# Optimization experiments

Hardware: AMD Instinct MI355X
Metric: run time of the kernel (lower is better)

## Reference

```python
import jax, jax.numpy as jnp
import numpy as np

EPS_MSG = 1e-7
EPS_BN = 1e-5


def _seg_softmax(logits, seg, num_segments):
    # logits: [E, D] per-edge logits; softmax over edges sharing the same dst node
    m = jax.ops.segment_max(logits, seg, num_segments=num_segments)
    m = jnp.where(jnp.isfinite(m), m, 0.0)
    e = jnp.exp(logits - m[seg])
    s = jax.ops.segment_sum(e, seg, num_segments=num_segments)
    return e / (s[seg] + 1e-16)


def _batchnorm(h, gamma, beta):
    mu = jnp.mean(h, axis=0)
    var = jnp.var(h, axis=0)
    return (h - mu) * jax.lax.rsqrt(var + EPS_BN) * gamma + beta


def setup_inputs() -> dict:
    key = jax.random.key(0)
    ks = jax.random.split(key, 12)
    N, E, G, D, L = 100000, 600000, 512, 128, 7
    x = jax.random.randint(ks[0], (N, 9), 0, 64, dtype=jnp.int32)
    edge_index = jax.random.randint(ks[1], (2, E), 0, N, dtype=jnp.int32)
    edge_attr = jax.random.randint(ks[2], (E, 3), 0, 8, dtype=jnp.int32)
    batch = jnp.sort(jax.random.randint(ks[3], (N,), 0, G, dtype=jnp.int32))
    rf_pred = jax.random.uniform(ks[4], (G,), dtype=jnp.float32)
    atom_emb = jax.random.normal(ks[5], (9, 64, D), dtype=jnp.float32) * 0.02
    bond_emb = jax.random.normal(ks[6], (3, 8, D), dtype=jnp.float32) * 0.02
    conv_w = jax.random.normal(ks[7], (L, D, D), dtype=jnp.float32) * 0.02
    conv_b = jnp.zeros((L, D), dtype=jnp.float32)
    ts = jnp.ones((L,), dtype=jnp.float32)  # learnable inverse temperatures (init 1/t style)
    gammas = jnp.ones((L, D), dtype=jnp.float32)
    bn_betas = jnp.zeros((L, D), dtype=jnp.float32)
    final_w = jax.random.normal(ks[8], (D, 1), dtype=jnp.float32) * 0.02
    final_b = jnp.zeros((1,), dtype=jnp.float32)
    beta = jnp.array([0.5], dtype=jnp.float32)
    return {"x": x, "edge_index": edge_index, "edge_attr": edge_attr, "batch": batch,
            "rf_pred": rf_pred, "atom_emb": atom_emb, "bond_emb": bond_emb,
            "conv_w": conv_w, "conv_b": conv_b, "ts": ts, "gammas": gammas,
            "bn_betas": bn_betas, "final_w": final_w, "final_b": final_b, "beta": beta}


def reference(x, edge_index, edge_attr, batch, rf_pred, atom_emb, bond_emb,
              conv_w, conv_b, ts, gammas, bn_betas, final_w, final_b, beta):
    N = x.shape[0]
    G = rf_pred.shape[0]
    L = conv_w.shape[0]
    src, dst = edge_index[0], edge_index[1]

    # AtomEncoder / BondEncoder: sum of per-feature embeddings
    h = jax.vmap(lambda tab, idx: tab[idx], in_axes=(0, 1))(atom_emb, x).sum(0)          # [N, D]
    e_emb = jax.vmap(lambda tab, idx: tab[idx], in_axes=(0, 1))(bond_emb, edge_attr).sum(0)  # [E, D]

    def genconv(l, hin):
        msg = jax.nn.relu(hin[src] + e_emb) + EPS_MSG          # [E, D]
        alpha = _seg_softmax(msg * ts[l], dst, N)              # softmax aggregation weights
        aggr = jax.ops.segment_sum(alpha * msg, dst, num_segments=N)  # [N, D]
        return (hin + aggr) @ conv_w[l] + conv_b[l]

    # res+ DeeperGCN
    h = genconv(0, h)
    for l in range(1, L):
        h2 = jax.nn.relu(_batchnorm(h, gammas[l - 1], bn_betas[l - 1]))
        h = genconv(l, h2) + h
    h = jax.nn.relu(_batchnorm(h, gammas[L - 1], bn_betas[L - 1]))

    # mean graph pooling
    counts = jnp.maximum(jax.ops.segment_sum(jnp.ones((N,), h.dtype), batch, num_segments=G), 1.0)
    hg = jax.ops.segment_sum(h, batch, num_segments=G) / counts[:, None]  # [G, D]

    dgcn_pred = hg @ final_w + final_b  # [G, 1]
    return (1.0 - beta) * jax.nn.sigmoid(dgcn_pred) + beta * rf_pred.reshape(-1, 1)
```

## Files before the change

### kernel.cpp

```cpp
#include <hip/hip_runtime.h>
#include <hip/hip_fp16.h>
#include <math.h>

#define D 128
#define PF 12

typedef _Float16 f16x8 __attribute__((ext_vector_type(8)));
typedef _Float16 f16x2 __attribute__((ext_vector_type(2)));
typedef float f32x4_t __attribute__((ext_vector_type(4)));

static __device__ __forceinline__ f16x2 h2v(__half2 h) {
    union { __half2 h; f16x2 v; } u; u.h = h; return u.v;
}
static __device__ __forceinline__ __half2 v2h(f16x2 v) {
    union { f16x2 v; __half2 h; } u; u.v = v; return u.h;
}


__global__ void hist_kernel(const int* __restrict__ edge_index, int* __restrict__ deg, int E) {
    int e = blockIdx.x * blockDim.x + threadIdx.x;
    if (e >= E) return;
    atomicAdd(&deg[edge_index[E + e]], 1);
}

__global__ void scanA_kernel(const int* __restrict__ deg, int* __restrict__ bsum, int n) {
    __shared__ int red[256];
    int b = blockIdx.x, t = threadIdx.x;
    int base = b * 1024 + t * 4;
    int s = 0;
#pragma unroll
    for (int j = 0; j < 4; ++j)
        if (base + j < n) s += deg[base + j];
    red[t] = s;
    __syncthreads();
    for (int off = 128; off > 0; off >>= 1) {
        if (t < off) red[t] += red[t + off];
        __syncthreads();
    }
    if (t == 0) bsum[b] = red[0];
}

__global__ void scanB_kernel(int* __restrict__ bsum, int nb) {
    __shared__ int sh[256];
    int t = threadIdx.x;
    sh[t] = (t < nb) ? bsum[t] : 0;
    __syncthreads();
    for (int off = 1; off < 256; off <<= 1) {
        int v = (t >= off) ? sh[t - off] : 0;
        __syncthreads();
        sh[t] += v;
        __syncthreads();
    }
    if (t < nb) bsum[t] = (t == 0) ? 0 : sh[t - 1];
}

__global__ void scanC_kernel(const int* __restrict__ deg, const int* __restrict__ boff,
                             int* __restrict__ row_start, int* __restrict__ cursor, int n) {
    __shared__ int sh[256];
    int b = blockIdx.x, t = threadIdx.x;
    int base = b * 1024 + t * 4;
    int v[4];
#pragma unroll
    for (int j = 0; j < 4; ++j) v[j] = (base + j < n) ? deg[base + j] : 0;
    int p[4];
    p[0] = 0; p[1] = v[0]; p[2] = v[0] + v[1]; p[3] = v[0] + v[1] + v[2];
    int s = p[3] + v[3];
    sh[t] = s;
    __syncthreads();
    for (int off = 1; off < 256; off <<= 1) {
        int x = (t >= off) ? sh[t - off] : 0;
        __syncthreads();
        sh[t] += x;
        __syncthreads();
    }
    int off0 = boff[b] + sh[t] - s;
#pragma unroll
    for (int j = 0; j < 4; ++j)
        if (base + j < n) {
            row_start[base + j] = off0 + p[j];
            cursor[base + j] = off0 + p[j];
        }
    if (base <= n - 1 && n - 1 < base + 4) row_start[n] = off0 + s;
}

__global__ void scatter_kernel(const int* __restrict__ edge_index, const int* __restrict__ edge_attr,
                               int* __restrict__ cursor, int2* __restrict__ csr, int E) {
    int e = blockIdx.x * blockDim.x + threadIdx.x;
    if (e >= E) return;
    int src = edge_index[e];
    int dst = edge_index[E + e];
    int pos = atomicAdd(&cursor[dst], 1);
    int a0 = edge_attr[e * 3], a1 = edge_attr[e * 3 + 1], a2 = edge_attr[e * 3 + 2];
    csr[pos] = make_int2(src, a0 | (a1 << 3) | (a2 << 6));
}

__global__ void misc_atom_kernel(const int* __restrict__ x, const float* __restrict__ atom_emb,
                                 _Float16* __restrict__ h16, int ndTotal,
                                 const float* __restrict__ bond_emb, __half2* __restrict__ evt,
                                 const float* __restrict__ conv_w, _Float16* __restrict__ wt,
                                 int wtTotal, const int* __restrict__ batch,
                                 int* __restrict__ gstart, int N, int G) {
    int idx = blockIdx.x * blockDim.x + threadIdx.x;
    if (idx < ndTotal) {
        int n = idx >> 7;
        int d = idx & 127;
        float acc = 0.f;
#pragma unroll
        for (int f = 0; f < 9; ++f) {
            int v = x[n * 9 + f];
            acc += atom_emb[(long long)(f * 64 + v) * D + d];
        }
        h16[idx] = (_Float16)acc;
        return;
    }
    idx -= ndTotal;
    if (idx < 512 * 64) {
        int combo = idx >> 6, j = idx & 63;
        int d0 = 2 * j;
        float ex = bond_emb[(combo & 7) * D + d0] +
                   bond_emb[(8 + ((combo >> 3) & 7)) * D + d0] +
                   bond_emb[(16 + ((combo >> 6) & 7)) * D + d0];
        float ey = bond_emb[(combo & 7) * D + d0 + 1] +
                   bond_emb[(8 + ((combo >> 3) & 7)) * D + d0 + 1] +
                   bond_emb[(16 + ((combo >> 6) & 7)) * D + d0 + 1];
        evt[idx] = __floats2half2_rn(ex, ey);
        return;
    }
    int widx = idx - 512 * 64;
    if (widx < wtTotal) {
        int l = widx >> 14;
        int rem = widx & 16383;
        int n = rem >> 7, k = rem & 127;
        wt[widx] = (_Float16)conv_w[(l << 14) + k * 128 + n];
        return;
    }
    int n = widx - wtTotal;
    if (n >= N) return;
    if (n == 0) {
        for (int g = 0; g <= batch[0]; ++g) gstart[g] = 0;
    } else {
        int b0 = batch[n - 1], b1 = batch[n];
        for (int g = b0 + 1; g <= b1; ++g) gstart[g] = n;
    }
    if (n == N - 1) {
        for (int g = batch[N - 1] + 1; g <= G; ++g) gstart[g] = N;
    }
}


__global__ void bn_stage1_kernel(const float* __restrict__ partial, int nb,
                                 float* __restrict__ p2) {
    int b = blockIdx.x, t = threadIdx.x;
    float acc = 0.f;
    for (int r = b; r < nb; r += 256)
        acc += partial[(long long)r * 256 + t];
    p2[b * 256 + t] = acc;
}

__global__ void bn_reduce_finalize_kernel(const float* __restrict__ partial, int nb,
                                          const float* __restrict__ gamma,
                                          const float* __restrict__ bnbeta, float invN,
                                          float* __restrict__ aArr, float* __restrict__ bArr) {
    __shared__ float r1[256], r2[256];
    int d = blockIdx.x, t = threadIdx.x;
    float a1 = 0.f, a2 = 0.f;
    for (int i = t; i < nb; i += 256) {
        a1 += partial[(long long)i * 256 + d];
        a2 += partial[(long long)i * 256 + 128 + d];
    }
    r1[t] = a1; r2[t] = a2;
    __syncthreads();
    for (int off = 128; off > 0; off >>= 1) {
        if (t < off) { r1[t] += r1[t + off]; r2[t] += r2[t + off]; }
        __syncthreads();
    }
    if (t == 0) {
        float mean = r1[0] * invN;
        float var = r2[0] * invN - mean * mean;
        float a = rsqrtf(var + 1e-5f) * gamma[d];
        aArr[d] = a;
        bArr[d] = bnbeta[d] - mean * a;
    }
}

__global__ __launch_bounds__(128, 8) void fused_layer_kernel(
        const __half2* __restrict__ h16c,
        const float* __restrict__ aArr, const float* __restrict__ bArr, int applyBN,
        const float* __restrict__ ts, int l,
        const int* __restrict__ row_start, const int2* __restrict__ csr,
        const __half2* __restrict__ evt,
        const _Float16* __restrict__ wt, const float* __restrict__ bias,
        int residual, _Float16* __restrict__ h16out,
        float* __restrict__ partial, int N) {
    __shared__ __align__(16) char smem[8192];
    _Float16* yh = (_Float16*)smem;
    __half2* tile2 = (__half2*)smem;

    int t = threadIdx.x;
    int row0 = blockIdx.x * 16;
    int wave = t >> 6;
    int lane = t & 63;
    float tsl = ts[l];
    int a = row0 + wave * 8;

    f16x2 zerov = (f16x2)(_Float16)0;
    f16x2 bnA2 = zerov, bnB2 = zerov;
    if (applyBN) {
        float2 af = ((const float2*)aArr)[lane];
        float2 bf = ((const float2*)bArr)[lane];
        bnA2[0] = (_Float16)af.x; bnA2[1] = (_Float16)af.y;
        bnB2[0] = (_Float16)bf.x; bnB2[1] = (_Float16)bf.y;
    }
    __half2 zero2 = v2h(zerov);

    int rsv = row_start[min(a + min(lane, 8), N)];
    __half2 hsv0 = zero2, hsv1 = zero2, hsv2 = zero2, hsv3 = zero2;
    __half2 hsv4 = zero2, hsv5 = zero2, hsv6 = zero2, hsv7 = zero2;
    if (a + 0 < N) hsv0 = h16c[(size_t)(a + 0) * 64 + lane];
    if (a + 1 < N) hsv1 = h16c[(size_t)(a + 1) * 64 + lane];
    if (a + 2 < N) hsv2 = h16c[(size_t)(a + 2) * 64 + lane];
    if (a + 3 < N) hsv3 = h16c[(size_t)(a + 3) * 64 + lane];
    if (a + 4 < N) hsv4 = h16c[(size_t)(a + 4) * 64 + lane];
    if (a + 5 < N) hsv5 = h16c[(size_t)(a + 5) * 64 + lane];
    if (a + 6 < N) hsv6 = h16c[(size_t)(a + 6) * 64 + lane];
    if (a + 7 < N) hsv7 = h16c[(size_t)(a + 7) * 64 + lane];

    int s0 = __builtin_amdgcn_readlane(rsv, 0);
    int s1 = __builtin_amdgcn_readlane(rsv, 8);

    int c0 = s0;
    int2 eaCur = make_int2(0, 0), eaNxt = make_int2(0, 0);
    if (c0 + lane < s1) eaCur = csr[c0 + lane];
    if (c0 + 64 + lane < s1) eaNxt = csr[c0 + 64 + lane];

    __half2 hvS[PF], evS[PF];
#pragma unroll
    for (int k = 0; k < PF; ++k) {
        int pp = s0 + k;
        if (pp < s1) {
            int srcp = __builtin_amdgcn_readlane(eaCur.x, k);
            int cbp = __builtin_amdgcn_readlane(eaCur.y, k);
            hvS[k] = h16c[(size_t)srcp * 64 + lane];
            evS[k] = evt[(size_t)cbp * 64 + lane];
        }
    }

    float accwx = 0.f, accwy = 0.f, accmx = 0.f, accmy = 0.f;
    int cur = 0;
    int nend = __builtin_amdgcn_readlane(rsv, 1);

#define CLOSE_ROW()                                                           \
    {                                                                         \
        __half2 hh;                                                           \
        switch (cur) {                                                        \
            case 0: hh = hsv0; break; case 1: hh = hsv1; break;               \
            case 2: hh = hsv2; break; case 3: hh = hsv3; break;               \
            case 4: hh = hsv4; break; case 5: hh = hsv5; break;               \
            case 6: hh = hsv6; break; default: hh = hsv7; break;              \
        }                                                                     \
        f16x2 hvv = h2v(hh);                                                  \
        if (applyBN)                                                          \
            hvv = __builtin_elementwise_max(hvv * bnA2 + bnB2, zerov);        \
        float2 yy;                                                            \
        yy.x = (float)hvv[0] + __fdividef(accmx, accwx + 1e-16f) + 1e-7f;     \
        yy.y = (float)hvv[1] + __fdividef(accmy, accwy + 1e-16f) + 1e-7f;     \
        tile2[(wave * 8 + cur) * 68 + lane] = __floats2half2_rn(yy.x, yy.y);  \
        accwx = accwy = accmx = accmy = 0.f;                                  \
        cur++;                                                                \
        nend = __builtin_amdgcn_readlane(rsv, min(cur + 1, 8));               \
    }

    while (cur < 8 && nend == s0) CLOSE_ROW();

    int total = s1 - s0;
    for (int it = 0; it < total; it += PF) {
#pragma unroll
        for (int k = 0; k < PF; ++k) {
            int p = s0 + it + k;
            if (p < s1) {
                f16x2 hv2 = h2v(hvS[k]);
                if (applyBN)
                    hv2 = __builtin_elementwise_max(hv2 * bnA2 + bnB2, zerov);
                f16x2 m2 = __builtin_elementwise_max(hv2 + h2v(evS[k]), zerov);
                float mx = (float)m2[0];
                float my = (float)m2[1];
                float wx = __expf(mx * tsl);
                float wy = __expf(my * tsl);
                accwx += wx; accmx = fmaf(wx, mx, accmx);
                accwy += wy; accmy = fmaf(wy, my, accmy);
                int pp = p + PF;
                if (pp < s1) {
                    if (pp >= c0 + 64) {
                        c0 += 64;
                        eaCur = eaNxt;
                        eaNxt = make_int2(0, 0);
                        if (c0 + 64 + lane < s1) eaNxt = csr[c0 + 64 + lane];
                    }
                    int q = pp - c0;
                    int srcp = __builtin_amdgcn_readlane(eaCur.x, q);
                    int cbp = __builtin_amdgcn_readlane(eaCur.y, q);
                    hvS[k] = h16c[(size_t)srcp * 64 + lane];
                    evS[k] = evt[(size_t)cbp * 64 + lane];
                }
                while (cur < 8 && nend == p + 1) CLOSE_ROW();
            }
        }
    }
#undef CLOSE_ROW
    __syncthreads();

    int ln = t & 15;
    int quad = (t & 63) >> 4;
    const _Float16* h16in = (const _Float16*)h16c;

    float cs[4] = {0.f, 0.f, 0.f, 0.f};
    float cq[4] = {0.f, 0.f, 0.f, 0.f};
    const _Float16* ap = yh + ln * 136 + quad * 8;
#pragma unroll
    for (int ct = 0; ct < 4; ++ct) {
        int colg = (wave * 4 + ct) * 16 + ln;
        const _Float16* bp = wt + (size_t)colg * 128 + quad * 8;
        f32x4_t c = {0.f, 0.f, 0.f, 0.f};
#pragma unroll
        for (int kk = 0; kk < 4; ++kk) {
            f16x8 av = *(const f16x8*)(ap + kk * 32);
            f16x8 bv = *(const f16x8*)(bp + kk * 32);
            c = __builtin_amdgcn_mfma_f32_16x16x32_f16(av, bv, c, 0, 0, 0);
        }
        float bsv = bias[colg];
#pragma unroll
        for (int reg = 0; reg < 4; ++reg) {
            int r = row0 + quad * 4 + reg;
            if (r < N) {
                long long off = (long long)r * D + colg;
                float o = c[reg] + bsv;
                if (residual) o += (float)h16in[off];
                h16out[off] = (_Float16)o;
                cs[ct] += o; cq[ct] += o * o;
            }
        }
    }

    __syncthreads();
    float* stats = (float*)smem;
    int grp = wave * 4 + quad;
#pragma unroll
    for (int ct = 0; ct < 4; ++ct) {
        int colg = (wave * 4 + ct) * 16 + ln;
        stats[grp * 256 + colg] = cs[ct];
        stats[grp * 256 + 128 + colg] = cq[ct];
    }
    __syncthreads();
    float ssumA = 0.f, ssumB = 0.f;
#pragma unroll
    for (int g = 0; g < 8; ++g) {
        ssumA += stats[g * 256 + t];
        ssumB += stats[g * 256 + 128 + t];
    }
    partial[(long long)blockIdx.x * 256 + t] = ssumA;
    partial[(long long)blockIdx.x * 256 + 128 + t] = ssumB;
}

__global__ void pool_head_kernel(const __half2* __restrict__ h16, const float* __restrict__ aArr,
                                 const float* __restrict__ bArr, const int* __restrict__ gstart,
                                 const float* __restrict__ fw, const float* __restrict__ fb,
                                 const float* __restrict__ beta, const float* __restrict__ rf,
                                 float* __restrict__ out) {
    __shared__ float redx[256], redy[256];
    int g = blockIdx.x, t = threadIdx.x;
    int d2 = t & 63, sub = t >> 6;
    int s0 = gstart[g], s1 = gstart[g + 1];
    float2 a2 = ((const float2*)aArr)[d2];
    float2 b2 = ((const float2*)bArr)[d2];
    float ax = 0.f, ay = 0.f;
    for (int n = s0 + sub; n < s1; n += 4) {
        f16x2 v = h2v(h16[(size_t)n * 64 + d2]);
        ax += fmaxf((float)v[0] * a2.x + b2.x, 0.f);
        ay += fmaxf((float)v[1] * a2.y + b2.y, 0.f);
    }
    redx[t] = ax; redy[t] = ay;
    __syncthreads();
    if (t < 64) {
        float sx = redx[t] + redx[t + 64] + redx[t + 128] + redx[t + 192];
        float sy = redy[t] + redy[t + 64] + redy[t + 128] + redy[t + 192];
        float v = sx * fw[2 * t] + sy * fw[2 * t + 1];
#pragma unroll
        for (int off = 32; off > 0; off >>= 1) v += __shfl_down(v, off);
        if (t == 0) {
            float c = fmaxf((float)(s1 - s0), 1.f);
            float pred = v / c + fb[0];
            float sig = 1.f / (1.f + __expf(-pred));
            float bb = beta[0];
            out[g] = (1.f - bb) * sig + bb * rf[g];
        }
    }
}

static inline size_t align16(size_t x) { return (x + 15) & ~(size_t)15; }

extern "C" void kernel_launch(void* const* d_in, const int* in_sizes, int n_in,
                              void* d_out, int out_size, void* d_ws, size_t ws_size,
                              hipStream_t stream) {
    const int* x = (const int*)d_in[0];
    const int* edge_index = (const int*)d_in[1];
    const int* edge_attr = (const int*)d_in[2];
    const int* batch = (const int*)d_in[3];
    const float* rf_pred = (const float*)d_in[4];
    const float* atom_emb = (const float*)d_in[5];
    const float* bond_emb = (const float*)d_in[6];
    const float* conv_w = (const float*)d_in[7];
    const float* conv_b = (const float*)d_in[8];
    const float* ts = (const float*)d_in[9];
    const float* gammas = (const float*)d_in[10];
    const float* bn_betas = (const float*)d_in[11];
    const float* final_w = (const float*)d_in[12];
    const float* final_b = (const float*)d_in[13];
    const float* beta = (const float*)d_in[14];
    float* out = (float*)d_out;

    int N = in_sizes[0] / 9;
    int E = in_sizes[1] / 2;
    int G = in_sizes[4];
    int L = in_sizes[9];

    int nTiles = (N + 15) / 16;
    size_t ND = (size_t)N * D;

    char* p = (char*)d_ws;
    _Float16* h16_a = (_Float16*)p;  p += align16(ND * 2);
    _Float16* h16_b = (_Float16*)p;  p += align16(ND * 2);
    __half2* evt = (__half2*)p;      p += align16((size_t)512 * 64 * 4);
    _Float16* wt = (_Float16*)p;     p += align16((size_t)L * 16384 * 2);
    float* partial = (float*)p;      p += align16((size_t)256 * nTiles * 4);
    float* p2 = (float*)p;           p += align16((size_t)256 * 256 * 4);
    float* aArr = (float*)p;         p += align16((size_t)D * 4);
    float* bArr = (float*)p;         p += align16((size_t)D * 4);
    int* gstart = (int*)p;           p += align16((size_t)(G + 1) * 4);
    int* deg = (int*)p;              p += align16((size_t)N * 4);
    int* row_start = (int*)p;        p += align16((size_t)(N + 1) * 4);
    int* cursor = (int*)p;           p += align16((size_t)N * 4);
    int* bsum = (int*)p;             p += align16((size_t)256 * 4);
    int2* csr = (int2*)p;            p += align16((size_t)E * 8);

    int eBlocks = (E + 255) / 256;
    int nb1024 = (N + 1023) / 1024;
    int wtTotal = L * 16384;
    int ndTotal = N * D;
    int miscTotal = ndTotal + 512 * 64 + wtTotal + N;
    int miscBlocks = (miscTotal + 255) / 256;
    float invN = 1.0f / (float)N;

    (void)hipMemsetAsync(deg, 0, (size_t)N * sizeof(int), stream);
    hist_kernel<<<eBlocks, 256, 0, stream>>>(edge_index, deg, E);
    scanA_kernel<<<nb1024, 256, 0, stream>>>(deg, bsum, N);
    scanB_kernel<<<1, 256, 0, stream>>>(bsum, nb1024);
    scanC_kernel<<<nb1024, 256, 0, stream>>>(deg, bsum, row_start, cursor, N);
    scatter_kernel<<<eBlocks, 256, 0, stream>>>(edge_index, edge_attr, cursor, csr, E);
    misc_atom_kernel<<<miscBlocks, 256, 0, stream>>>(x, atom_emb, h16_a, ndTotal,
                                                     bond_emb, evt, conv_w, wt, wtTotal,
                                                     batch, gstart, N, G);

    _Float16* h16c = h16_a;
    _Float16* h16n = h16_b;
    for (int l = 0; l < L; ++l) {
        int applyBN = (l >= 1) ? 1 : 0;
        if (applyBN) {
            bn_stage1_kernel<<<256, 256, 0, stream>>>(partial, nTiles, p2);
            bn_reduce_finalize_kernel<<<128, 256, 0, stream>>>(
                p2, 256, gammas + (size_t)(l - 1) * D,
                bn_betas + (size_t)(l - 1) * D, invN, aArr, bArr);
        }
        fused_layer_kernel<<<nTiles, 128, 0, stream>>>(
            (const __half2*)h16c, aArr, bArr, applyBN, ts, l, row_start, csr, evt,
            wt + (size_t)l * 16384, conv_b + (size_t)l * D,
            applyBN, h16n, partial, N);
        _Float16* tmp16 = h16c; h16c = h16n; h16n = tmp16;
    }

    bn_stage1_kernel<<<256, 256, 0, stream>>>(partial, nTiles, p2);
    bn_reduce_finalize_kernel<<<128, 256, 0, stream>>>(
        p2, 256, gammas + (size_t)(L - 1) * D,
        bn_betas + (size_t)(L - 1) * D, invN, aArr, bArr);
    pool_head_kernel<<<G, 256, 0, stream>>>((const __half2*)h16c, aArr, bArr, gstart,
                                            final_w, final_b, beta, rf_pred, out);
}
```

Before: 789.8 us.

## Cut kernel launches: fuse scans, scatter+misc, atomic BN stat accumulation

Folds the single-block scan of block sums into scanC, merges the CSR scatter with the atom/bond/weight prep kernel, and replaces the two-stage BN partial reduction with atomic accumulation into four striped per-layer accumulators. A tiny finalize kernel (or pool_head itself for the last layer) then turns these into the BN scale and shift. The goal is to remove launch overhead and the partial-buffer round trips. In exchange it adds float atomics, which make the sum order nondeterministic and can contend on the accumulators. It also relies on the single memset covering the contiguous acc and deg regions.

```diff
diff --git a/kernel.cpp b/kernel.cpp
--- a/kernel.cpp
+++ b/kernel.cpp
@@ -40,24 +40,13 @@
     if (t == 0) bsum[b] = red[0];
 }
 
-__global__ void scanB_kernel(int* __restrict__ bsum, int nb) {
+__global__ void scanC_kernel(const int* __restrict__ deg, const int* __restrict__ bsum,
+                             int nb, int* __restrict__ row_start, int* __restrict__ cursor,
+                             int n) {
     __shared__ int sh[256];
-    int t = threadIdx.x;
-    sh[t] = (t < nb) ? bsum[t] : 0;
-    __syncthreads();
-    for (int off = 1; off < 256; off <<= 1) {
-        int v = (t >= off) ? sh[t - off] : 0;
-        __syncthreads();
-        sh[t] += v;
-        __syncthreads();
-    }
-    if (t < nb) bsum[t] = (t == 0) ? 0 : sh[t - 1];
-}
-
-__global__ void scanC_kernel(const int* __restrict__ deg, const int* __restrict__ boff,
-                             int* __restrict__ row_start, int* __restrict__ cursor, int n) {
-    __shared__ int sh[256];
+    __shared__ int sb[256];
     int b = blockIdx.x, t = threadIdx.x;
+    sb[t] = (t < nb) ? bsum[t] : 0;
     int base = b * 1024 + t * 4;
     int v[4];
 #pragma unroll
@@ -69,11 +58,14 @@
     __syncthreads();
     for (int off = 1; off < 256; off <<= 1) {
         int x = (t >= off) ? sh[t - off] : 0;
+        int y = (t >= off) ? sb[t - off] : 0;
         __syncthreads();
         sh[t] += x;
+        sb[t] += y;
         __syncthreads();
     }
-    int off0 = boff[b] + sh[t] - s;
+    int boffb = (b == 0) ? 0 : sb[b - 1];
+    int off0 = boffb + sh[t] - s;
 #pragma unroll
     for (int j = 0; j < 4; ++j)
         if (base + j < n) {
@@ -83,24 +75,25 @@
     if (base <= n - 1 && n - 1 < base + 4) row_start[n] = off0 + s;
 }
 
-__global__ void scatter_kernel(const int* __restrict__ edge_index, const int* __restrict__ edge_attr,
-                               int* __restrict__ cursor, int2* __restrict__ csr, int E) {
-    int e = blockIdx.x * blockDim.x + threadIdx.x;
-    if (e >= E) return;
-    int src = edge_index[e];
-    int dst = edge_index[E + e];
-    int pos = atomicAdd(&cursor[dst], 1);
-    int a0 = edge_attr[e * 3], a1 = edge_attr[e * 3 + 1], a2 = edge_attr[e * 3 + 2];
-    csr[pos] = make_int2(src, a0 | (a1 << 3) | (a2 << 6));
-}
-
-__global__ void misc_atom_kernel(const int* __restrict__ x, const float* __restrict__ atom_emb,
-                                 _Float16* __restrict__ h16, int ndTotal,
-                                 const float* __restrict__ bond_emb, __half2* __restrict__ evt,
-                                 const float* __restrict__ conv_w, _Float16* __restrict__ wt,
-                                 int wtTotal, const int* __restrict__ batch,
-                                 int* __restrict__ gstart, int N, int G) {
+__global__ void scatter_misc_kernel(const int* __restrict__ edge_index,
+                                    const int* __restrict__ edge_attr,
+                                    int* __restrict__ cursor, int2* __restrict__ csr, int E,
+                                    const int* __restrict__ x, const float* __restrict__ atom_emb,
+                                    _Float16* __restrict__ h16, int ndTotal,
+                                    const float* __restrict__ bond_emb, __half2* __restrict__ evt,
+                                    const float* __restrict__ conv_w, _Float16* __restrict__ wt,
+                                    int wtTotal, const int* __restrict__ batch,
+                                    int* __restrict__ gstart, int N, int G) {
     int idx = blockIdx.x * blockDim.x + threadIdx.x;
+    if (idx < E) {
+        int src = edge_index[idx];
+        int dst = edge_index[E + idx];
+        int pos = atomicAdd(&cursor[dst], 1);
+        int a0 = edge_attr[idx * 3], a1 = edge_attr[idx * 3 + 1], a2 = edge_attr[idx * 3 + 2];
+        csr[pos] = make_int2(src, a0 | (a1 << 3) | (a2 << 6));
+        return;
+    }
+    idx -= E;
     if (idx < ndTotal) {
         int n = idx >> 7;
         int d = idx & 127;
@@ -148,39 +141,18 @@
 }
 
 
-__global__ void bn_stage1_kernel(const float* __restrict__ partial, int nb,
-                                 float* __restrict__ p2) {
-    int b = blockIdx.x, t = threadIdx.x;
-    float acc = 0.f;
-    for (int r = b; r < nb; r += 256)
-        acc += partial[(long long)r * 256 + t];
-    p2[b * 256 + t] = acc;
-}
-
-__global__ void bn_reduce_finalize_kernel(const float* __restrict__ partial, int nb,
-                                          const float* __restrict__ gamma,
-                                          const float* __restrict__ bnbeta, float invN,
-                                          float* __restrict__ aArr, float* __restrict__ bArr) {
-    __shared__ float r1[256], r2[256];
-    int d = blockIdx.x, t = threadIdx.x;
-    float a1 = 0.f, a2 = 0.f;
-    for (int i = t; i < nb; i += 256) {
-        a1 += partial[(long long)i * 256 + d];
-        a2 += partial[(long long)i * 256 + 128 + d];
-    }
-    r1[t] = a1; r2[t] = a2;
-    __syncthreads();
-    for (int off = 128; off > 0; off >>= 1) {
-        if (t < off) { r1[t] += r1[t + off]; r2[t] += r2[t + off]; }
-        __syncthreads();
-    }
-    if (t == 0) {
-        float mean = r1[0] * invN;
-        float var = r2[0] * invN - mean * mean;
-        float a = rsqrtf(var + 1e-5f) * gamma[d];
-        aArr[d] = a;
-        bArr[d] = bnbeta[d] - mean * a;
-    }
+__global__ void bn_finalize_kernel(const float* __restrict__ acc4,
+                                   const float* __restrict__ gamma,
+                                   const float* __restrict__ bnbeta, float invN,
+                                   float* __restrict__ aArr, float* __restrict__ bArr) {
+    int t = threadIdx.x;
+    float s1 = acc4[t] + acc4[256 + t] + acc4[512 + t] + acc4[768 + t];
+    float s2 = acc4[128 + t] + acc4[384 + t] + acc4[640 + t] + acc4[896 + t];
+    float mean = s1 * invN;
+    float var = s2 * invN - mean * mean;
+    float a = rsqrtf(var + 1e-5f) * gamma[t];
+    aArr[t] = a;
+    bArr[t] = bnbeta[t] - mean * a;
 }
 
 __global__ __launch_bounds__(128, 8) void fused_layer_kernel(
@@ -191,7 +163,7 @@
         const __half2* __restrict__ evt,
         const _Float16* __restrict__ wt, const float* __restrict__ bias,
         int residual, _Float16* __restrict__ h16out,
-        float* __restrict__ partial, int N) {
+        float* __restrict__ accL, int N) {
     __shared__ __align__(16) char smem[8192];
     _Float16* yh = (_Float16*)smem;
     __half2* tile2 = (__half2*)smem;
@@ -357,21 +329,36 @@
         ssumA += stats[g * 256 + t];
         ssumB += stats[g * 256 + 128 + t];
     }
-    partial[(long long)blockIdx.x * 256 + t] = ssumA;
-    partial[(long long)blockIdx.x * 256 + 128 + t] = ssumB;
-}
-
-__global__ void pool_head_kernel(const __half2* __restrict__ h16, const float* __restrict__ aArr,
-                                 const float* __restrict__ bArr, const int* __restrict__ gstart,
+    int cbase = (blockIdx.x & 3) << 8;
+    atomicAdd(&accL[cbase + t], ssumA);
+    atomicAdd(&accL[cbase + 128 + t], ssumB);
+}
+
+__global__ void pool_head_kernel(const __half2* __restrict__ h16,
+                                 const float* __restrict__ acc4,
+                                 const float* __restrict__ gamma,
+                                 const float* __restrict__ bnbeta, float invN,
+                                 const int* __restrict__ gstart,
                                  const float* __restrict__ fw, const float* __restrict__ fb,
                                  const float* __restrict__ beta, const float* __restrict__ rf,
                                  float* __restrict__ out) {
     __shared__ float redx[256], redy[256];
+    __shared__ float sA[128], sB[128];
     int g = blockIdx.x, t = threadIdx.x;
+    if (t < 128) {
+        float s1 = acc4[t] + acc4[256 + t] + acc4[512 + t] + acc4[768 + t];
+        float s2 = acc4[128 + t] + acc4[384 + t] + acc4[640 + t] + acc4[896 + t];
+        float mean = s1 * invN;
+        float var = s2 * invN - mean * mean;
+        float a = rsqrtf(var + 1e-5f) * gamma[t];
+        sA[t] = a;
+        sB[t] = bnbeta[t] - mean * a;
+    }
+    __syncthreads();
     int d2 = t & 63, sub = t >> 6;
     int s0 = gstart[g], s1 = gstart[g + 1];
-    float2 a2 = ((const float2*)aArr)[d2];
-    float2 b2 = ((const float2*)bArr)[d2];
+    float2 a2 = make_float2(sA[2 * d2], sA[2 * d2 + 1]);
+    float2 b2 = make_float2(sB[2 * d2], sB[2 * d2 + 1]);
     float ax = 0.f, ay = 0.f;
     for (int n = s0 + sub; n < s1; n += 4) {
         f16x2 v = h2v(h16[(size_t)n * 64 + d2]);
@@ -425,17 +412,17 @@
 
     int nTiles = (N + 15) / 16;
     size_t ND = (size_t)N * D;
+    size_t accFloats = (size_t)L * 1024;
 
     char* p = (char*)d_ws;
     _Float16* h16_a = (_Float16*)p;  p += align16(ND * 2);
     _Float16* h16_b = (_Float16*)p;  p += align16(ND * 2);
     __half2* evt = (__half2*)p;      p += align16((size_t)512 * 64 * 4);
     _Float16* wt = (_Float16*)p;     p += align16((size_t)L * 16384 * 2);
-    float* partial = (float*)p;      p += align16((size_t)256 * nTiles * 4);
-    float* p2 = (float*)p;           p += align16((size_t)256 * 256 * 4);
     float* aArr = (float*)p;         p += align16((size_t)D * 4);
     float* bArr = (float*)p;         p += align16((size_t)D * 4);
     int* gstart = (int*)p;           p += align16((size_t)(G + 1) * 4);
+    float* acc = (float*)p;          p += align16(accFloats * 4);
     int* deg = (int*)p;              p += align16((size_t)N * 4);
     int* row_start = (int*)p;        p += align16((size_t)(N + 1) * 4);
     int* cursor = (int*)p;           p += align16((size_t)N * 4);
@@ -446,41 +433,37 @@
     int nb1024 = (N + 1023) / 1024;
     int wtTotal = L * 16384;
     int ndTotal = N * D;
-    int miscTotal = ndTotal + 512 * 64 + wtTotal + N;
-    int miscBlocks = (miscTotal + 255) / 256;
+    int smTotal = E + ndTotal + 512 * 64 + wtTotal + N;
+    int smBlocks = (smTotal + 255) / 256;
     float invN = 1.0f / (float)N;
 
-    (void)hipMemsetAsync(deg, 0, (size_t)N * sizeof(int), stream);
+    (void)hipMemsetAsync(acc, 0, align16(accFloats * 4) + (size_t)N * 4, stream);
     hist_kernel<<<eBlocks, 256, 0, stream>>>(edge_index, deg, E);
     scanA_kernel<<<nb1024, 256, 0, stream>>>(deg, bsum, N);
-    scanB_kernel<<<1, 256, 0, stream>>>(bsum, nb1024);
-    scanC_kernel<<<nb1024, 256, 0, stream>>>(deg, bsum, row_start, cursor, N);
-    scatter_kernel<<<eBlocks, 256, 0, stream>>>(edge_index, edge_attr, cursor, csr, E);
-    misc_atom_kernel<<<miscBlocks, 256, 0, stream>>>(x, atom_emb, h16_a, ndTotal,
-                                                     bond_emb, evt, conv_w, wt, wtTotal,
-                                                     batch, gstart, N, G);
+    scanC_kernel<<<nb1024, 256, 0, stream>>>(deg, bsum, nb1024, row_start, cursor, N);
+    scatter_misc_kernel<<<smBlocks, 256, 0, stream>>>(edge_index, edge_attr, cursor, csr, E,
+                                                      x, atom_emb, h16_a, ndTotal,
+                                                      bond_emb, evt, conv_w, wt, wtTotal,
+                                                      batch, gstart, N, G);
 
     _Float16* h16c = h16_a;
     _Float16* h16n = h16_b;
     for (int l = 0; l < L; ++l) {
         int applyBN = (l >= 1) ? 1 : 0;
         if (applyBN) {
-            bn_stage1_kernel<<<256, 256, 0, stream>>>(partial, nTiles, p2);
-            bn_reduce_finalize_kernel<<<128, 256, 0, stream>>>(
-                p2, 256, gammas + (size_t)(l - 1) * D,
+            bn_finalize_kernel<<<1, 128, 0, stream>>>(
+                acc + (size_t)(l - 1) * 1024, gammas + (size_t)(l - 1) * D,
                 bn_betas + (size_t)(l - 1) * D, invN, aArr, bArr);
         }
         fused_layer_kernel<<<nTiles, 128, 0, stream>>>(
             (const __half2*)h16c, aArr, bArr, applyBN, ts, l, row_start, csr, evt,
             wt + (size_t)l * 16384, conv_b + (size_t)l * D,
-            applyBN, h16n, partial, N);
+            applyBN, h16n, acc + (size_t)l * 1024, N);
         _Float16* tmp16 = h16c; h16c = h16n; h16n = tmp16;
     }
 
-    bn_stage1_kernel<<<256, 256, 0, stream>>>(partial, nTiles, p2);
-    bn_reduce_finalize_kernel<<<128, 256, 0, stream>>>(
-        p2, 256, gammas + (size_t)(L - 1) * D,
-        bn_betas + (size_t)(L - 1) * D, invN, aArr, bArr);
-    pool_head_kernel<<<G, 256, 0, stream>>>((const __half2*)h16c, aArr, bArr, gstart,
-                                            final_w, final_b, beta, rf_pred, out);
-}
+    pool_head_kernel<<<G, 256, 0, stream>>>(
+        (const __half2*)h16c, acc + (size_t)(L - 1) * 1024,
+        gammas + (size_t)(L - 1) * D, bn_betas + (size_t)(L - 1) * D, invN,
+        gstart, final_w, final_b, beta, rf_pred, out);
+}
```

Result: slower. 847.7 us (+7.3%).
